# Kernel tuning notes

Measured on AMD Instinct MI355X. Metric: run time of the kernel, lower is better.

## Reference

```python
import jax, jax.numpy as jnp
import numpy as np

N_NODES = 100000
N_EDGES = 640000
D_IN = 128
D_OUT = 128


def setup_inputs() -> dict:
    key = jax.random.key(0)
    k_x, k_w, k_v, k_r, k_c = jax.random.split(key, 5)
    x = jax.random.normal(k_x, (N_NODES, D_IN), dtype=jnp.float32)
    # Xavier-uniform init for weights, zeros for bias (matches module init)
    limit = float(np.sqrt(6.0 / (D_IN + D_OUT)))
    weights = jax.random.uniform(k_w, (D_IN, D_OUT), dtype=jnp.float32,
                                 minval=-limit, maxval=limit)
    bias = jnp.zeros((D_OUT,), dtype=jnp.float32)
    # Sparse normalized adjacency in COO form: value[e] * y[col[e]] scattered to row[e]
    edge_val = jax.random.uniform(k_v, (N_EDGES,), dtype=jnp.float32)
    row = jax.random.randint(k_r, (N_EDGES,), 0, N_NODES, dtype=jnp.int32)
    col = jax.random.randint(k_c, (N_EDGES,), 0, N_NODES, dtype=jnp.int32)
    return {"x": x, "weights": weights, "bias": bias,
            "edge_val": edge_val, "row": row, "col": col}


def reference(x, weights, bias, edge_val, row, col):
    # y = x @ W  (dense GEMM)  [N, D_OUT]
    y = x @ weights
    # SpMM: out[i] = sum_{e: row[e]==i} edge_val[e] * y[col[e]]
    msg = edge_val[:, None] * y[col]            # [E, D_OUT] irregular gather
    agg = jax.ops.segment_sum(msg, row, num_segments=x.shape[0])
    return agg + bias
```

## Files before the change

### kernel.cpp

```cpp
#include <hip/hip_runtime.h>
#include <hip/hip_bf16.h>


#define N_NODES 100000
#define N_EDGES 640000
#define D 128
#define ELL_K 16
#define OVF_CAP 8192

typedef __attribute__((ext_vector_type(8))) short short8;
typedef __attribute__((ext_vector_type(4))) float f32x4;
typedef __attribute__((ext_vector_type(4))) ushort us4;

__device__ __forceinline__ ushort f2bf(float f) {
    uint u = __float_as_uint(f);
    u += 0x7fff + ((u >> 16) & 1);
    return (ushort)(u >> 16);
}
__device__ __forceinline__ float bflo(uint u) { return __uint_as_float(u << 16); }
__device__ __forceinline__ float bfhi(uint u) { return __uint_as_float(u & 0xffff0000u); }

__global__ __launch_bounds__(256, 2) void gemm_xw(const float* __restrict__ x,
                                                  const float* __restrict__ w,
                                                  ushort* __restrict__ y,
                                                  int* __restrict__ counts,
                                                  int* __restrict__ ovfCnt) {
    __shared__ ushort wt[128 * 128];
    const int tid = threadIdx.x;

    int gz = blockIdx.x * 256 + tid;
    if (gz < N_NODES) counts[gz] = 0;
    if (gz == 0) *ovfCnt = 0;

    #pragma unroll
    for (int it = 0; it < 16; ++it) {
        int idx4 = tid + it * 256;
        int k = idx4 >> 5;
        int n0 = (idx4 & 31) * 4;
        float4 v = *(const float4*)(w + (size_t)idx4 * 4);
        float vv[4] = {v.x, v.y, v.z, v.w};
        #pragma unroll
        for (int q = 0; q < 4; ++q) {
            int n = n0 + q;
            wt[n * 128 + (k ^ ((n & 7) << 3))] = f2bf(vv[q]);
        }
    }
    __syncthreads();

    const int lane = tid & 63;
    const int l15 = lane & 15;
    const int h = lane >> 4;

    short8 bfr[8][4];
    #pragma unroll
    for (int j = 0; j < 8; ++j) {
        int n = 16 * j + l15;
        #pragma unroll
        for (int ks = 0; ks < 4; ++ks) {
            int k0 = 32 * ks + 8 * h;
            bfr[j][ks] = *(const short8*)&wt[n * 128 + (k0 ^ ((n & 7) << 3))];
        }
    }

    const int waveGlobal = blockIdx.x * 4 + (tid >> 6);
    const int nWaves = gridDim.x * 4;
    const int nTiles = N_NODES / 16;

    for (int t = waveGlobal; t < nTiles; t += nWaves) {
        const float* xr = x + (size_t)(t * 16 + l15) * D;
        float4 xb[8];
        #pragma unroll
        for (int ks = 0; ks < 4; ++ks) {
            xb[2 * ks]     = *(const float4*)(xr + 32 * ks + 8 * h);
            xb[2 * ks + 1] = *(const float4*)(xr + 32 * ks + 8 * h + 4);
        }
        f32x4 acc[8];
        #pragma unroll
        for (int j = 0; j < 8; ++j) acc[j] = (f32x4){0.f, 0.f, 0.f, 0.f};
        #pragma unroll
        for (int ks = 0; ks < 4; ++ks) {
            const float* p0 = (const float*)&xb[2 * ks];
            const float* p1 = (const float*)&xb[2 * ks + 1];
            short8 a;
            a[0] = f2bf(p0[0]); a[1] = f2bf(p0[1]); a[2] = f2bf(p0[2]); a[3] = f2bf(p0[3]);
            a[4] = f2bf(p1[0]); a[5] = f2bf(p1[1]); a[6] = f2bf(p1[2]); a[7] = f2bf(p1[3]);
            #pragma unroll
            for (int j = 0; j < 8; ++j)
                acc[j] = __builtin_amdgcn_mfma_f32_16x16x32_bf16(bfr[j][ks], a, acc[j], 0, 0, 0);
        }
        ushort* yn = y + (size_t)(t * 16 + l15) * D;
        #pragma unroll
        for (int j = 0; j < 8; ++j) {
            us4 o;
            o.x = f2bf(acc[j][0]); o.y = f2bf(acc[j][1]);
            o.z = f2bf(acc[j][2]); o.w = f2bf(acc[j][3]);
            *(us4*)(yn + 16 * j + 4 * h) = o;
        }
    }
}

__global__ void scatter_ell(const float* __restrict__ ev, const int* __restrict__ row,
                            const int* __restrict__ col, int* __restrict__ counts,
                            float2* __restrict__ es, int* __restrict__ ovfCnt,
                            int* __restrict__ ovfRow, int* __restrict__ ovfCol,
                            float* __restrict__ ovfVal) {
    int i = blockIdx.x * 256 + threadIdx.x;
    if (i >= N_EDGES) return;
    int r = row[i];
    int p = atomicAdd(&counts[r], 1);
    if (p < ELL_K) {
        float2 e;
        e.x = ev[i];
        e.y = __int_as_float(col[i]);
        es[r * ELL_K + p] = e;
    } else {
        int q = atomicAdd(ovfCnt, 1);
        if (q < OVF_CAP) {
            ovfRow[q] = r;
            ovfCol[q] = col[i];
            ovfVal[q] = ev[i];
        }
    }
}

__global__ __launch_bounds__(256) void spmm_ell(const ushort* __restrict__ y,
                                                const float2* __restrict__ es,
                                                const int* __restrict__ counts,
                                                const float* __restrict__ bias,
                                                float* __restrict__ out) {
    const int tid = threadIdx.x;
    const int lane = tid & 63;
    const int wid = blockIdx.x * 4 + (tid >> 6);
    const float2 b2 = *(const float2*)(bias + lane * 2);

    #pragma unroll 1
    for (int rep = 0; rep < 2; ++rep) {
        const int n = __builtin_amdgcn_readfirstlane(wid * 2 + rep);
        int deg = counts[n];
        if (deg > ELL_K) deg = ELL_K;
        const float4* er = (const float4*)(es + (size_t)n * ELL_K);

        float ax = 0.f, ay = 0.f;
        #pragma unroll
        for (int g = 0; g < 4; ++g) {
            if (4 * g < deg) {
                float4 sA = er[2 * g];
                float4 sB = er[2 * g + 1];
                int c0 = __float_as_int(sA.y);
                int c1 = (4 * g + 1 < deg) ? __float_as_int(sA.w) : c0;
                int c2 = (4 * g + 2 < deg) ? __float_as_int(sB.y) : c0;
                int c3 = (4 * g + 3 < deg) ? __float_as_int(sB.w) : c0;
                uint u0 = *(const uint*)(y + ((size_t)c0 << 7) + lane * 2);
                uint u1 = *(const uint*)(y + ((size_t)c1 << 7) + lane * 2);
                uint u2 = *(const uint*)(y + ((size_t)c2 << 7) + lane * 2);
                uint u3 = *(const uint*)(y + ((size_t)c3 << 7) + lane * 2);
                float v0 = sA.x;
                float v1 = (4 * g + 1 < deg) ? sA.z : 0.f;
                float v2 = (4 * g + 2 < deg) ? sB.x : 0.f;
                float v3 = (4 * g + 3 < deg) ? sB.z : 0.f;
                ax += v0 * bflo(u0); ay += v0 * bfhi(u0);
                ax += v1 * bflo(u1); ay += v1 * bfhi(u1);
                ax += v2 * bflo(u2); ay += v2 * bfhi(u2);
                ax += v3 * bflo(u3); ay += v3 * bfhi(u3);
            }
        }
        float2 o = {ax + b2.x, ay + b2.y};
        *(float2*)(out + ((size_t)n << 7) + lane * 2) = o;
    }
}

__global__ void ovf_fix(const ushort* __restrict__ y, const int* __restrict__ ovfRow,
                        const int* __restrict__ ovfCol, const float* __restrict__ ovfVal,
                        const int* __restrict__ ovfCnt, float* __restrict__ out) {
    int nOvf = *ovfCnt;
    if (nOvf > OVF_CAP) nOvf = OVF_CAP;
    int total = nOvf * 32;
    for (int idx = blockIdx.x * 256 + threadIdx.x; idx < total; idx += gridDim.x * 256) {
        int e = idx >> 5;
        int c = idx & 31;
        int r = ovfRow[e];
        int col = ovfCol[e];
        float v = ovfVal[e];
        uint2 u = *(const uint2*)(y + ((size_t)col << 7) + c * 4);
        atomicAdd(&out[(size_t)r * D + c * 4 + 0], v * bflo(u.x));
        atomicAdd(&out[(size_t)r * D + c * 4 + 1], v * bfhi(u.x));
        atomicAdd(&out[(size_t)r * D + c * 4 + 2], v * bflo(u.y));
        atomicAdd(&out[(size_t)r * D + c * 4 + 3], v * bfhi(u.y));
    }
}

extern "C" void kernel_launch(void* const* d_in, const int* in_sizes, int n_in,
                              void* d_out, int out_size, void* d_ws, size_t ws_size,
                              hipStream_t stream) {
    const float* x = (const float*)d_in[0];
    const float* w = (const float*)d_in[1];
    const float* bias = (const float*)d_in[2];
    const float* ev = (const float*)d_in[3];
    const int* row = (const int*)d_in[4];
    const int* col = (const int*)d_in[5];
    float* out = (float*)d_out;

    size_t off = 0;
    auto carve = [&](size_t bytes) -> void* {
        void* p = (char*)d_ws + off;
        off += (bytes + 255) & ~(size_t)255;
        return p;
    };
    ushort* y = (ushort*)carve((size_t)N_NODES * D * sizeof(ushort));
    int* counts = (int*)carve((size_t)N_NODES * sizeof(int));
    float2* es = (float2*)carve((size_t)N_NODES * ELL_K * sizeof(float2));
    int* ovfCnt = (int*)carve(sizeof(int));
    int* ovfRow = (int*)carve(OVF_CAP * sizeof(int));
    int* ovfCol = (int*)carve(OVF_CAP * sizeof(int));
    float* ovfVal = (float*)carve(OVF_CAP * sizeof(float));

    gemm_xw<<<512, 256, 0, stream>>>(x, w, y, counts, ovfCnt);
    scatter_ell<<<(N_EDGES + 255) / 256, 256, 0, stream>>>(ev, row, col, counts, es,
                                                           ovfCnt, ovfRow, ovfCol, ovfVal);
    spmm_ell<<<N_NODES / 8, 256, 0, stream>>>(y, es, counts, bias, out);
    ovf_fix<<<16, 256, 0, stream>>>(y, ovfRow, ovfCol, ovfVal, ovfCnt, out);
}
```

Baseline: 92.07 us.

## Build ELL via two-pass bucketed partition with shared-memory assembly

Replaces the per-edge global atomic scatter into the ELL array with a two-level approach. Edges are first partitioned into 256-row buckets using shared-memory histograms and one global atomic per bucket per chunk. Each bucket's ELL slots are then assembled in shared memory and written out with coalesced stores. This is meant to cut random global atomics and scattered writes, at the cost of an extra kernel launch and an intermediate buffer pass. Bucket overflow beyond BCAP is routed to the existing overflow path.

After: 85.75 us. -6.9%, faster.

```diff
diff --git a/kernel.cpp b/kernel.cpp
--- a/kernel.cpp
+++ b/kernel.cpp
@@ -7,6 +7,10 @@
 #define D 128
 #define ELL_K 16
 #define OVF_CAP 8192
+#define NB 391
+#define BCAP 2048
+#define CHUNK 4096
+#define NCHUNKS 157
 
 typedef __attribute__((ext_vector_type(8))) short short8;
 typedef __attribute__((ext_vector_type(4))) float f32x4;
@@ -23,13 +27,13 @@
 __global__ __launch_bounds__(256, 2) void gemm_xw(const float* __restrict__ x,
                                                   const float* __restrict__ w,
                                                   ushort* __restrict__ y,
-                                                  int* __restrict__ counts,
+                                                  int* __restrict__ bucketCursor,
                                                   int* __restrict__ ovfCnt) {
     __shared__ ushort wt[128 * 128];
     const int tid = threadIdx.x;
 
     int gz = blockIdx.x * 256 + tid;
-    if (gz < N_NODES) counts[gz] = 0;
+    if (gz < NB) bucketCursor[gz] = gz * BCAP;
     if (gz == 0) *ovfCnt = 0;
 
     #pragma unroll
@@ -99,28 +103,110 @@
     }
 }
 
-__global__ void scatter_ell(const float* __restrict__ ev, const int* __restrict__ row,
-                            const int* __restrict__ col, int* __restrict__ counts,
-                            float2* __restrict__ es, int* __restrict__ ovfCnt,
-                            int* __restrict__ ovfRow, int* __restrict__ ovfCol,
-                            float* __restrict__ ovfVal) {
-    int i = blockIdx.x * 256 + threadIdx.x;
-    if (i >= N_EDGES) return;
-    int r = row[i];
-    int p = atomicAdd(&counts[r], 1);
-    if (p < ELL_K) {
-        float2 e;
-        e.x = ev[i];
-        e.y = __int_as_float(col[i]);
-        es[r * ELL_K + p] = e;
-    } else {
-        int q = atomicAdd(ovfCnt, 1);
-        if (q < OVF_CAP) {
-            ovfRow[q] = r;
-            ovfCol[q] = col[i];
-            ovfVal[q] = ev[i];
-        }
-    }
+__global__ __launch_bounds__(256) void partition_edges(const float* __restrict__ ev,
+                                                       const int* __restrict__ row,
+                                                       const int* __restrict__ col,
+                                                       int* __restrict__ bucketCursor,
+                                                       uint2* __restrict__ es0,
+                                                       int* __restrict__ ovfCnt,
+                                                       int* __restrict__ ovfRow,
+                                                       int* __restrict__ ovfCol,
+                                                       float* __restrict__ ovfVal) {
+    __shared__ int hist[NB];
+    __shared__ int cur[NB];
+    const int tid = threadIdx.x;
+    const int base = blockIdx.x * CHUNK;
+
+    for (int t = tid; t < NB; t += 256) hist[t] = 0;
+    __syncthreads();
+
+    #pragma unroll
+    for (int it = 0; it < CHUNK / 256; ++it) {
+        int i = base + it * 256 + tid;
+        if (i < N_EDGES) atomicAdd(&hist[row[i] >> 8], 1);
+    }
+    __syncthreads();
+
+    for (int t = tid; t < NB; t += 256) {
+        int hcnt = hist[t];
+        cur[t] = (hcnt > 0) ? atomicAdd(&bucketCursor[t], hcnt) : 0;
+    }
+    __syncthreads();
+
+    #pragma unroll
+    for (int it = 0; it < CHUNK / 256; ++it) {
+        int i = base + it * 256 + tid;
+        if (i < N_EDGES) {
+            int r = row[i];
+            int b = r >> 8;
+            int p = atomicAdd(&cur[b], 1);
+            if (p < (b + 1) * BCAP) {
+                uint2 e;
+                e.x = __float_as_uint(ev[i]);
+                e.y = (uint)col[i] | ((uint)(r & 255) << 20);
+                es0[p] = e;
+            } else {
+                int q = atomicAdd(ovfCnt, 1);
+                if (q < OVF_CAP) {
+                    ovfRow[q] = r;
+                    ovfCol[q] = col[i];
+                    ovfVal[q] = ev[i];
+                }
+            }
+        }
+    }
+}
+
+__global__ __launch_bounds__(256) void build_ell(const uint2* __restrict__ es0,
+                                                 const int* __restrict__ bucketCursor,
+                                                 float2* __restrict__ es,
+                                                 int* __restrict__ counts,
+                                                 int* __restrict__ ovfCnt,
+                                                 int* __restrict__ ovfRow,
+                                                 int* __restrict__ ovfCol,
+                                                 float* __restrict__ ovfVal) {
+    __shared__ float2 ell[256 * ELL_K];
+    __shared__ int lcnt[256];
+    const int tid = threadIdx.x;
+    const int b = blockIdx.x;
+
+    lcnt[tid] = 0;
+    __syncthreads();
+
+    int cnt = bucketCursor[b] - b * BCAP;
+    if (cnt > BCAP) cnt = BCAP;
+    const uint2* src = es0 + (size_t)b * BCAP;
+
+    for (int i = tid; i < cnt; i += 256) {
+        uint2 e = src[i];
+        int r = e.y >> 20;
+        int p = atomicAdd(&lcnt[r], 1);
+        if (p < ELL_K) {
+            float2 rec;
+            rec.x = __uint_as_float(e.x);
+            rec.y = __uint_as_float(e.y & 0xFFFFFu);
+            ell[r * ELL_K + p] = rec;
+        } else {
+            int q = atomicAdd(ovfCnt, 1);
+            if (q < OVF_CAP) {
+                ovfRow[q] = b * 256 + r;
+                ovfCol[q] = (int)(e.y & 0xFFFFFu);
+                ovfVal[q] = __uint_as_float(e.x);
+            }
+        }
+    }
+    __syncthreads();
+
+    const int nbase = b * 256;
+    int nvalid = N_NODES - nbase;
+    if (nvalid > 256) nvalid = 256;
+
+    if (tid < nvalid) counts[nbase + tid] = lcnt[tid];
+
+    float4* dst4 = (float4*)(es + (size_t)nbase * ELL_K);
+    const float4* ell4 = (const float4*)ell;
+    for (int t = tid; t < nvalid * (ELL_K / 2); t += 256)
+        dst4[t] = ell4[t];
 }
 
 __global__ __launch_bounds__(256) void spmm_ell(const ushort* __restrict__ y,
@@ -209,14 +295,18 @@
     ushort* y = (ushort*)carve((size_t)N_NODES * D * sizeof(ushort));
     int* counts = (int*)carve((size_t)N_NODES * sizeof(int));
     float2* es = (float2*)carve((size_t)N_NODES * ELL_K * sizeof(float2));
+    uint2* es0 = (uint2*)carve((size_t)NB * BCAP * sizeof(uint2));
+    int* bucketCursor = (int*)carve(NB * sizeof(int));
     int* ovfCnt = (int*)carve(sizeof(int));
     int* ovfRow = (int*)carve(OVF_CAP * sizeof(int));
     int* ovfCol = (int*)carve(OVF_CAP * sizeof(int));
     float* ovfVal = (float*)carve(OVF_CAP * sizeof(float));
 
-    gemm_xw<<<512, 256, 0, stream>>>(x, w, y, counts, ovfCnt);
-    scatter_ell<<<(N_EDGES + 255) / 256, 256, 0, stream>>>(ev, row, col, counts, es,
-                                                           ovfCnt, ovfRow, ovfCol, ovfVal);
+    gemm_xw<<<512, 256, 0, stream>>>(x, w, y, bucketCursor, ovfCnt);
+    partition_edges<<<NCHUNKS, 256, 0, stream>>>(ev, row, col, bucketCursor, es0,
+                                                 ovfCnt, ovfRow, ovfCol, ovfVal);
+    build_ell<<<NB, 256, 0, stream>>>(es0, bucketCursor, es, counts,
+                                      ovfCnt, ovfRow, ovfCol, ovfVal);
     spmm_ell<<<N_NODES / 8, 256, 0, stream>>>(y, es, counts, bias, out);
     ovf_fix<<<16, 256, 0, stream>>>(y, ovfRow, ovfCol, ovfVal, ovfCnt, out);
 }
```
